# Kernel optimization log

Measured on AMD Instinct MI355X. Metric: run time of the kernel, lower is better.

The kernel has to match this reference:

```python
import jax, jax.numpy as jnp
import numpy as np

B, N, H = 4, 4096, 1024
NH, HD, M = 16, 64, 256
EPS = 1e-5


def gaussian_orthogonal(m, d, rng):
    # scaling=0: rows are orthogonal blocks scaled by norms of fresh gaussian rows
    blocks = []
    n_blocks = (m + d - 1) // d
    for _ in range(n_blocks):
        q, _ = np.linalg.qr(rng.standard_normal((d, d)))
        blocks.append(q.T)
    mat = np.concatenate(blocks, 0)[:m]
    multiplier = np.linalg.norm(rng.standard_normal((m, d)), axis=1)
    return (multiplier[:, None] * mat).astype(np.float32)


def setup_inputs():
    key = jax.random.key(0)
    keys = iter(jax.random.split(key, 24))
    rng = np.random.default_rng(0)

    def w(din, dout):
        return jax.random.normal(next(keys), (din, dout), jnp.float32) * 0.02

    inp = {
        'x': jax.random.normal(next(keys), (B, N, H), jnp.float32),
        'enc_outputs': jax.random.normal(next(keys), (B, N, H), jnp.float32),
    }
    for p in ('sa', 'ca'):
        for q in ('wq', 'wk', 'wv', 'wo'):
            inp[f'{p}_{q}'] = w(H, H)
            inp[f'{p}_b{q[1]}'] = jnp.zeros((H,), jnp.float32)
        inp[f'{p}_proj'] = jnp.asarray(gaussian_orthogonal(M, HD, rng))
    inp['ff_w1'] = w(H, 4 * H); inp['ff_b1'] = jnp.zeros((4 * H,), jnp.float32)
    inp['ff_w2'] = w(4 * H, H); inp['ff_b2'] = jnp.zeros((H,), jnp.float32)
    for i in (1, 2, 3):
        inp[f'ln{i}_g'] = jnp.ones((H,), jnp.float32)
        inp[f'ln{i}_b'] = jnp.zeros((H,), jnp.float32)
    return inp


def _split(t):
    b, n, _ = t.shape
    return t.reshape(b, n, NH, HD).transpose(0, 2, 1, 3)  # [b,h,n,d]


def _feat(data, proj):
    # FAVOR+ nonnegative softmax kernel features
    dn = HD ** -0.25
    dd = jnp.einsum('bhnd,md->bhnm', data * dn, proj)
    diag = 0.5 * (dn ** 2) * jnp.sum(data * data, -1)  # [b,h,n]
    dd = dd - diag[..., None] - jnp.max(dd, axis=-1, keepdims=True)
    return (M ** -0.5) * (jnp.exp(dd) + 1e-4)


def _attn(q, k, v, wq, bq, wk, bk, wv, bv, wo, bo, proj):
    b, n, _ = q.shape
    Q = _split(q @ wq + bq)
    K = _split(k @ wk + bk)
    V = _split(v @ wv + bv)
    Qp = _feat(Q, proj)  # [b,h,n,m]
    Kp = _feat(K, proj)
    denom = jnp.einsum('bhnm,bhm->bhn', Qp, Kp.sum(2))[..., None]
    ctx = jnp.einsum('bhnm,bhnd->bhmd', Kp, V)          # O(N) linear attention
    out = jnp.einsum('bhnm,bhmd->bhnd', Qp, ctx) / denom
    # faithful to torch .view(B,-1,hidden) WITHOUT head transpose-back
    out = out.reshape(b, -1, H)
    return out @ wo + bo


def _ln(x, g, b):
    mu = jnp.mean(x, -1, keepdims=True)
    var = jnp.mean((x - mu) ** 2, -1, keepdims=True)
    return (x - mu) / jnp.sqrt(var + EPS) * g + b


def reference(x, enc_outputs, sa_wq, sa_bq, sa_wk, sa_bk, sa_wv, sa_bv, sa_wo, sa_bo,
              sa_proj, ca_wq, ca_bq, ca_wk, ca_bk, ca_wv, ca_bv, ca_wo, ca_bo, ca_proj,
              ff_w1, ff_b1, ff_w2, ff_b2, ln1_g, ln1_b, ln2_g, ln2_b, ln3_g, ln3_b):
    h = _ln(x + _attn(x, x, x, sa_wq, sa_bq, sa_wk, sa_bk, sa_wv, sa_bv, sa_wo, sa_bo, sa_proj), ln1_g, ln1_b)
    h = _ln(h + _attn(h, enc_outputs, enc_outputs, ca_wq, ca_bq, ca_wk, ca_bk, ca_wv, ca_bv, ca_wo, ca_bo, ca_proj), ln2_g, ln2_b)
    ff = jax.nn.gelu(h @ ff_w1 + ff_b1, approximate=True) @ ff_w2 + ff_b2  # dropout prob 0 -> identity
    return _ln(h + ff, ln3_g, ln3_b)
```

## Files before the change

kernel.cpp:

```cpp
#include <hip/hip_runtime.h>
#include <hip/hip_bf16.h>

#define B_ 4
#define N_ 4096
#define H_ 1024
#define NH_ 16
#define HD_ 64
#define M_ 256

typedef __attribute__((ext_vector_type(8))) __bf16 bf16x8;
typedef __attribute__((ext_vector_type(4))) float f32x4;
typedef __attribute__((ext_vector_type(4))) unsigned int u32x4;

__device__ __forceinline__ float bf2f(unsigned short u) {
  union { unsigned int i; float f; } x; x.i = ((unsigned int)u) << 16; return x.f;
}
__device__ __forceinline__ unsigned short f2b(float f) {
  __hip_bfloat16 h = __float2bfloat16(f);
  return *(unsigned short*)&h;
}
__device__ __forceinline__ float gelu_f(float x) {
  const float c = 0.7978845608028654f;
  float t = tanhf(c * (x + 0.044715f * x * x * x));
  return 0.5f * x * (1.0f + t);
}

typedef __attribute__((address_space(3))) unsigned int as3_uint;
typedef const __attribute__((address_space(1))) unsigned int as1_uint;
__device__ __forceinline__ void gload16(const void* g, void* l) {
  __builtin_amdgcn_global_load_lds((as1_uint*)g, (as3_uint*)l, 16, 0, 0);
}

template<int ACT>
__launch_bounds__(256)
__global__ void gemm_mfma(const unsigned short* __restrict__ A, int lda,
                          const unsigned short* __restrict__ BT,
                          const float* __restrict__ bias,
                          unsigned short* __restrict__ C, int ldc, int K) {
  __shared__ __align__(16) char LDS[65536];

  const int tid = threadIdx.x;
  const int nwg = gridDim.x * gridDim.y;
  const int lin = blockIdx.y * gridDim.x + blockIdx.x;
  const int mm = (lin & 7) * (nwg >> 3) + (lin >> 3);
  const int bx = mm % gridDim.x, by = mm / gridDim.x;
  const int row0 = by * 128;
  const int col0 = bx * 128;

  const int w = tid >> 6, lane = tid & 63;
  const int wm = w >> 1, wn = w & 1;
  const int ln = lane & 15, hi = lane >> 4;
  const int rswz = (ln & 7) << 4;

  const int srow = w * 8 + (lane >> 3);
  const int schunk = ((lane & 7) ^ (lane >> 3)) * 8;
  const unsigned short* Ag = A + (long long)(row0 + srow) * lda + schunk;
  const unsigned short* Bg = BT + (long long)(col0 + srow) * K + schunk;
  const int ldsw = w * 1024;

  f32x4 acc[4][4];
#pragma unroll
  for (int i = 0; i < 4; ++i)
#pragma unroll
    for (int j = 0; j < 4; ++j) acc[i][j] = (f32x4){0.f, 0.f, 0.f, 0.f};

  auto STAGE = [&](int p, int k0) {
    char* dst = LDS + p * 32768 + ldsw;
#pragma unroll
    for (int i = 0; i < 4; ++i) {
      gload16(Ag + (long long)i * 32 * lda + k0, dst + i * 4096);
      gload16(Bg + (long long)i * 32 * K + k0, dst + 16384 + i * 4096);
    }
  };
  auto COMPUTE = [&](int p) {
    char* AsB = LDS + p * 32768;
    char* BsB = AsB + 16384;
#pragma unroll
    for (int kc = 0; kc < 2; ++kc) {
      const int koff = (kc * 64 + hi * 16) ^ rswz;
      bf16x8 av[4], bv[4];
#pragma unroll
      for (int i = 0; i < 4; ++i)
        av[i] = *(bf16x8*)(AsB + (wm * 64 + i * 16 + ln) * 128 + koff);
#pragma unroll
      for (int j = 0; j < 4; ++j)
        bv[j] = *(bf16x8*)(BsB + (wn * 64 + j * 16 + ln) * 128 + koff);
#pragma unroll
      for (int i = 0; i < 4; ++i)
#pragma unroll
        for (int j = 0; j < 4; ++j)
          acc[i][j] = __builtin_amdgcn_mfma_f32_16x16x32_bf16(av[i], bv[j], acc[i][j], 0, 0, 0);
    }
  };

  STAGE(0, 0);
  __syncthreads();
  int cur = 0;
  for (int k0 = 64; k0 < K; k0 += 64) {
    STAGE(cur ^ 1, k0);
    COMPUTE(cur);
    __syncthreads();
    cur ^= 1;
  }
  COMPUTE(cur);
  __syncthreads();

  char* SB = LDS;
#pragma unroll
  for (int j = 0; j < 4; ++j) {
    const int lcol = wn * 64 + j * 16 + ln;
    const float bj = bias ? bias[col0 + lcol] : 0.0f;
#pragma unroll
    for (int i = 0; i < 4; ++i) {
      const int rb_ = wm * 64 + i * 16 + hi * 4;
#pragma unroll
      for (int r = 0; r < 4; ++r) {
        float v = acc[i][j][r] + bj;
        if (ACT == 1) v = gelu_f(v);
        const int row = rb_ + r;
        *(unsigned short*)(SB + ((row * 256 + lcol * 2) ^ ((row & 7) << 4))) = f2b(v);
      }
    }
  }
  __syncthreads();
#pragma unroll
  for (int p = 0; p < 8; ++p) {
    const int idx = p * 256 + tid;
    const int row = idx >> 4, seg = idx & 15;
    u32x4 v = *(u32x4*)(SB + ((row * 256 + seg * 16) ^ ((row & 7) << 4)));
    __builtin_nontemporal_store(v, (u32x4*)(C + (long long)(row0 + row) * ldc + col0 + seg * 8));
  }
}

__launch_bounds__(256)
__global__ void ctxksum_mfma(const unsigned short* __restrict__ QKV,
                             const unsigned short* __restrict__ pjB,
                             float* __restrict__ ksumP,
                             float* __restrict__ ctxP) {
  __shared__ char Kt[8192];
  __shared__ char Vt[8192];
  __shared__ char Pt[32768];
  __shared__ float rmaxL[4][64];
  __shared__ float ssqL[64];
  const int z = blockIdx.z, b = z >> 4, hh = z & 15;
  const int sp = blockIdx.x;
  const int n0 = sp * 512;
  const unsigned short* Kg = QKV + (long long)(b * 4096) * 3072 + 1024 + hh * 64;
  const unsigned short* Vg = QKV + (long long)(b * 4096) * 3072 + 2048 + hh * 64;
  const int tid = threadIdx.x;
  const int w = tid >> 6, lane = tid & 63;
  const int ln = lane & 15, hi = lane >> 4;
  const int rswz = (ln & 7) << 4;

  f32x4 accC[4][4];
#pragma unroll
  for (int i = 0; i < 4; ++i)
#pragma unroll
    for (int j = 0; j < 4; ++j) accC[i][j] = (f32x4){0.f, 0.f, 0.f, 0.f};
  float cs[4] = {0.f, 0.f, 0.f, 0.f};

  for (int t = 0; t < 8; ++t) {
    const long long nt = n0 + t * 64;
    __syncthreads();
#pragma unroll
    for (int p = 0; p < 2; ++p) {
      int id = p * 256 + tid;
      int r = id >> 3, c = id & 7;
      gload16(Kg + (nt + r) * 3072 + ((c ^ (r & 7)) * 8), Kt + id * 16);
    }
    {
      int n = tid >> 2, d0 = (tid & 3) * 16;
      const unsigned short* src = Vg + (nt + n) * 3072 + d0;
      ushort4 v0 = *(const ushort4*)src;
      ushort4 v1 = *(const ushort4*)(src + 4);
      ushort4 v2 = *(const ushort4*)(src + 8);
      ushort4 v3 = *(const ushort4*)(src + 12);
      unsigned short vals[16] = {v0.x, v0.y, v0.z, v0.w, v1.x, v1.y, v1.z, v1.w,
                                 v2.x, v2.y, v2.z, v2.w, v3.x, v3.y, v3.z, v3.w};
#pragma unroll
      for (int e = 0; e < 16; ++e) {
        int d = d0 + e;
        *(unsigned short*)(Vt + ((d * 128 + n * 2) ^ ((d & 7) << 4))) = vals[e];
      }
    }
    __syncthreads();

    f32x4 accF[4][4];
#pragma unroll
    for (int i = 0; i < 4; ++i)
#pragma unroll
      for (int j = 0; j < 4; ++j) accF[i][j] = (f32x4){0.f, 0.f, 0.f, 0.f};
#pragma unroll
    for (int kc = 0; kc < 2; ++kc) {
      const int koff = (kc * 64 + hi * 16) ^ rswz;
      bf16x8 av[4], bq[4];
#pragma unroll
      for (int i = 0; i < 4; ++i)
        av[i] = *(bf16x8*)(Kt + (i * 16 + ln) * 128 + koff);
#pragma unroll
      for (int j = 0; j < 4; ++j)
        bq[j] = *(const bf16x8*)(pjB + (w * 64 + j * 16 + ln) * 64 + kc * 32 + hi * 8);
#pragma unroll
      for (int i = 0; i < 4; ++i)
#pragma unroll
        for (int j = 0; j < 4; ++j)
          accF[i][j] = __builtin_amdgcn_mfma_f32_16x16x32_bf16(av[i], bq[j], accF[i][j], 0, 0, 0);
    }

#pragma unroll
    for (int i = 0; i < 4; ++i)
#pragma unroll
      for (int r = 0; r < 4; ++r) {
        float m = fmaxf(fmaxf(accF[i][0][r], accF[i][1][r]), fmaxf(accF[i][2][r], accF[i][3][r]));
        m = fmaxf(m, __shfl_xor(m, 1, 64));
        m = fmaxf(m, __shfl_xor(m, 2, 64));
        m = fmaxf(m, __shfl_xor(m, 4, 64));
        m = fmaxf(m, __shfl_xor(m, 8, 64));
        if (ln == 0) rmaxL[w][i * 16 + hi * 4 + r] = m;
      }
    {
      int r = tid >> 2, q = tid & 3;
      int b0 = (r * 128 + q * 32) ^ ((r & 7) << 4);
      int b1 = (r * 128 + q * 32 + 16) ^ ((r & 7) << 4);
      u32x4 x0 = *(u32x4*)(Kt + b0);
      u32x4 x1 = *(u32x4*)(Kt + b1);
      float s = 0.f;
#pragma unroll
      for (int e = 0; e < 4; ++e) {
        float a0 = bf2f((unsigned short)(x0[e] & 0xffff)), a1 = bf2f((unsigned short)(x0[e] >> 16));
        float a2 = bf2f((unsigned short)(x1[e] & 0xffff)), a3 = bf2f((unsigned short)(x1[e] >> 16));
        s += a0 * a0 + a1 * a1 + a2 * a2 + a3 * a3;
      }
      s += __shfl_xor(s, 1, 64);
      s += __shfl_xor(s, 2, 64);
      if (q == 0) ssqL[r] = s;
    }
    __syncthreads();

    float base[4][4];
#pragma unroll
    for (int i = 0; i < 4; ++i)
#pragma unroll
      for (int r = 0; r < 4; ++r) {
        int row = i * 16 + hi * 4 + r;
        base[i][r] = 0.0625f * ssqL[row] +
                     fmaxf(fmaxf(rmaxL[0][row], rmaxL[1][row]), fmaxf(rmaxL[2][row], rmaxL[3][row]));
      }
#pragma unroll
    for (int i = 0; i < 4; ++i)
#pragma unroll
      for (int j = 0; j < 4; ++j) {
        ushort4 pk;
        pk.x = f2b(0.0625f * (expf(accF[i][j][0] - base[i][0]) + 1e-4f));
        pk.y = f2b(0.0625f * (expf(accF[i][j][1] - base[i][1]) + 1e-4f));
        pk.z = f2b(0.0625f * (expf(accF[i][j][2] - base[i][2]) + 1e-4f));
        pk.w = f2b(0.0625f * (expf(accF[i][j][3] - base[i][3]) + 1e-4f));
        cs[j] += bf2f(pk.x) + bf2f(pk.y) + bf2f(pk.z) + bf2f(pk.w);
        int m = w * 64 + j * 16 + ln;
        *(ushort4*)(Pt + ((m * 128 + i * 32 + hi * 8) ^ ((m & 7) << 4))) = pk;
      }
    __syncthreads();

#pragma unroll
    for (int kc = 0; kc < 2; ++kc) {
      const int koff = (kc * 64 + hi * 16) ^ rswz;
      bf16x8 am[4], bv[4];
#pragma unroll
      for (int i = 0; i < 4; ++i)
        am[i] = *(bf16x8*)(Pt + (w * 64 + i * 16 + ln) * 128 + koff);
#pragma unroll
      for (int j = 0; j < 4; ++j)
        bv[j] = *(bf16x8*)(Vt + (j * 16 + ln) * 128 + koff);
#pragma unroll
      for (int i = 0; i < 4; ++i)
#pragma unroll
        for (int j = 0; j < 4; ++j)
          accC[i][j] = __builtin_amdgcn_mfma_f32_16x16x32_bf16(am[i], bv[j], accC[i][j], 0, 0, 0);
    }
  }

#pragma unroll
  for (int j = 0; j < 4; ++j) {
    cs[j] += __shfl_xor(cs[j], 16, 64);
    cs[j] += __shfl_xor(cs[j], 32, 64);
  }
  if (hi == 0) {
#pragma unroll
    for (int j = 0; j < 4; ++j)
      ksumP[((long long)z * 8 + sp) * 256 + w * 64 + j * 16 + ln] = cs[j];
  }

  float* ctxPs = ctxP + ((long long)z * 8 + sp) * 16384;
#pragma unroll
  for (int dh = 0; dh < 2; ++dh) {
    __syncthreads();
#pragma unroll
    for (int i = 0; i < 4; ++i)
#pragma unroll
      for (int jj = 0; jj < 2; ++jj) {
        int j = dh * 2 + jj;
#pragma unroll
        for (int r = 0; r < 4; ++r) {
          int m = w * 64 + i * 16 + hi * 4 + r;
          int dl = jj * 16 + ln;
          *(float*)(Pt + ((m * 128 + dl * 4) ^ ((m & 7) << 4))) = accC[i][j][r];
        }
      }
    __syncthreads();
#pragma unroll
    for (int p = 0; p < 8; ++p) {
      int idx = p * 256 + tid;
      int row = idx >> 3, seg = idx & 7;
      u32x4 v = *(u32x4*)(Pt + ((row * 128 + seg * 16) ^ ((row & 7) << 4)));
      __builtin_nontemporal_store(v, (u32x4*)(ctxPs + dh * 8192 + row * 32 + seg * 4));
    }
  }
}

__launch_bounds__(256)
__global__ void ctx_fin(const float* __restrict__ ctxP, const float* __restrict__ ksumP,
                        unsigned short* __restrict__ ctxbf, float* __restrict__ ksumF) {
  __shared__ float acc[16384];
  const int z = blockIdx.x;
  const int tid = threadIdx.x;
  const float* base = ctxP + (long long)z * 8 * 16384;
  for (int i = tid; i < 16384; i += 256) {
    float s = 0.f;
#pragma unroll
    for (int q = 0; q < 8; ++q) s += base[(long long)q * 16384 + i];
    acc[i] = s;
  }
  {
    const float* kb = ksumP + (long long)z * 8 * 256;
    float s = 0.f;
#pragma unroll
    for (int q = 0; q < 8; ++q) s += kb[q * 256 + tid];
    ksumF[z * 256 + tid] = s;
  }
  __syncthreads();
  unsigned short* dst = ctxbf + (long long)z * 16384;
  for (int cc = tid; cc < 2048; cc += 256) {
    int mh = cc >> 10, rem = cc & 1023, d = rem >> 4, cl = rem & 15;
    int m0 = mh * 128 + cl * 8;
    int dh = d >> 5, dl = d & 31;
    ushort4 o0, o1;
    o0.x = f2b(acc[dh * 8192 + (m0 + 0) * 32 + dl]);
    o0.y = f2b(acc[dh * 8192 + (m0 + 1) * 32 + dl]);
    o0.z = f2b(acc[dh * 8192 + (m0 + 2) * 32 + dl]);
    o0.w = f2b(acc[dh * 8192 + (m0 + 3) * 32 + dl]);
    o1.x = f2b(acc[dh * 8192 + (m0 + 4) * 32 + dl]);
    o1.y = f2b(acc[dh * 8192 + (m0 + 5) * 32 + dl]);
    o1.z = f2b(acc[dh * 8192 + (m0 + 6) * 32 + dl]);
    o1.w = f2b(acc[dh * 8192 + (m0 + 7) * 32 + dl]);
    unsigned short* p = dst + (long long)mh * 8192 + (d * 16 + (cl ^ (d & 7))) * 8;
    *(ushort4*)p = o0;
    *(ushort4*)(p + 4) = o1;
  }
}

__launch_bounds__(256)
__global__ void ao_fused(const unsigned short* __restrict__ QKV,
                         const unsigned short* __restrict__ pjB,
                         const float* __restrict__ ksum,
                         const unsigned short* __restrict__ ctxbf,
                         unsigned short* __restrict__ AO) {
  __shared__ char Qt[8192];
  __shared__ char Ps[32768];
  __shared__ char Ch[32768];
  __shared__ float rmaxL[4][64];
  __shared__ float ssqL[64];
  __shared__ float dprt[4][64];
  __shared__ float denomS[64];
  const int z = blockIdx.z, b = z >> 4, hh = z & 15;
  const int n0 = blockIdx.x * 64;
  const unsigned short* Qg = QKV + (long long)(b * 4096) * 3072 + hh * 64;
  const int tid = threadIdx.x;
  const int w = tid >> 6, lane = tid & 63;
  const int ln = lane & 15, hi = lane >> 4;
  const int rswz = (ln & 7) << 4;

#pragma unroll
  for (int p = 0; p < 8; ++p) {
    int id = p * 256 + tid;
    gload16(ctxbf + (long long)z * 16384 + id * 8, Ch + id * 16);
  }
#pragma unroll
  for (int p = 0; p < 2; ++p) {
    int id = p * 256 + tid;
    int r = id >> 3, c = id & 7;
    gload16(Qg + (long long)(n0 + r) * 3072 + ((c ^ (r & 7)) * 8), Qt + id * 16);
  }
  __syncthreads();

  f32x4 accF[4][4];
#pragma unroll
  for (int i = 0; i < 4; ++i)
#pragma unroll
    for (int j = 0; j < 4; ++j) accF[i][j] = (f32x4){0.f, 0.f, 0.f, 0.f};
#pragma unroll
  for (int kc = 0; kc < 2; ++kc) {
    const int koff = (kc * 64 + hi * 16) ^ rswz;
    bf16x8 av[4], bq[4];
#pragma unroll
    for (int i = 0; i < 4; ++i)
      av[i] = *(bf16x8*)(Qt + (i * 16 + ln) * 128 + koff);
#pragma unroll
    for (int j = 0; j < 4; ++j)
      bq[j] = *(const bf16x8*)(pjB + (w * 64 + j * 16 + ln) * 64 + kc * 32 + hi * 8);
#pragma unroll
    for (int i = 0; i < 4; ++i)
#pragma unroll
      for (int j = 0; j < 4; ++j)
        accF[i][j] = __builtin_amdgcn_mfma_f32_16x16x32_bf16(av[i], bq[j], accF[i][j], 0, 0, 0);
  }

#pragma unroll
  for (int i = 0; i < 4; ++i)
#pragma unroll
    for (int r = 0; r < 4; ++r) {
      float m = fmaxf(fmaxf(accF[i][0][r], accF[i][1][r]), fmaxf(accF[i][2][r], accF[i][3][r]));
      m = fmaxf(m, __shfl_xor(m, 1, 64));
      m = fmaxf(m, __shfl_xor(m, 2, 64));
      m = fmaxf(m, __shfl_xor(m, 4, 64));
      m = fmaxf(m, __shfl_xor(m, 8, 64));
      if (ln == 0) rmaxL[w][i * 16 + hi * 4 + r] = m;
    }
  {
    int r = tid >> 2, q = tid & 3;
    int b0 = (r * 128 + q * 32) ^ ((r & 7) << 4);
    int b1 = (r * 128 + q * 32 + 16) ^ ((r & 7) << 4);
    u32x4 x0 = *(u32x4*)(Qt + b0);
    u32x4 x1 = *(u32x4*)(Qt + b1);
    float s = 0.f;
#pragma unroll
    for (int e = 0; e < 4; ++e) {
      float a0 = bf2f((unsigned short)(x0[e] & 0xffff)), a1 = bf2f((unsigned short)(x0[e] >> 16));
      float a2 = bf2f((unsigned short)(x1[e] & 0xffff)), a3 = bf2f((unsigned short)(x1[e] >> 16));
      s += a0 * a0 + a1 * a1 + a2 * a2 + a3 * a3;
    }
    s += __shfl_xor(s, 1, 64);
    s += __shfl_xor(s, 2, 64);
    if (q == 0) ssqL[r] = s;
  }
  __syncthreads();

  float ks[4];
#pragma unroll
  for (int j = 0; j < 4; ++j) ks[j] = ksum[z * 256 + w * 64 + j * 16 + ln];
#pragma unroll
  for (int i = 0; i < 4; ++i)
#pragma unroll
    for (int r = 0; r < 4; ++r) {
      int n = i * 16 + hi * 4 + r;
      float base = 0.0625f * ssqL[n] +
                   fmaxf(fmaxf(rmaxL[0][n], rmaxL[1][n]), fmaxf(rmaxL[2][n], rmaxL[3][n]));
      float dp = 0.f;
#pragma unroll
      for (int j = 0; j < 4; ++j) {
        float v = 0.0625f * (expf(accF[i][j][r] - base) + 1e-4f);
        unsigned short vb = f2b(v);
        int m = w * 64 + j * 16 + ln;
        *(unsigned short*)(Ps + n * 512 + ((m * 2) ^ ((n & 7) << 4))) = vb;
        dp += bf2f(vb) * ks[j];
      }
      dp += __shfl_xor(dp, 1, 64);
      dp += __shfl_xor(dp, 2, 64);
      dp += __shfl_xor(dp, 4, 64);
      dp += __shfl_xor(dp, 8, 64);
      if (ln == 0) dprt[w][n] = dp;
    }
  __syncthreads();
  if (tid < 64) denomS[tid] = dprt[0][tid] + dprt[1][tid] + dprt[2][tid] + dprt[3][tid];

  f32x4 accO[4];
#pragma unroll
  for (int j = 0; j < 4; ++j) accO[j] = (f32x4){0.f, 0.f, 0.f, 0.f};
#pragma unroll
  for (int mh = 0; mh < 2; ++mh) {
#pragma unroll
    for (int ms = 0; ms < 4; ++ms) {
      const int koff = (ms * 64 + hi * 16);
      bf16x8 ap = *(bf16x8*)(Ps + (w * 16 + ln) * 512 + ((mh * 256 + koff) ^ rswz));
      bf16x8 bc[4];
#pragma unroll
      for (int j = 0; j < 4; ++j)
        bc[j] = *(bf16x8*)(Ch + mh * 16384 + (j * 16 + ln) * 256 + (koff ^ rswz));
#pragma unroll
      for (int j = 0; j < 4; ++j)
        accO[j] = __builtin_amdgcn_mfma_f32_16x16x32_bf16(ap, bc[j], accO[j], 0, 0, 0);
    }
  }
  __syncthreads();

  float inv[4];
#pragma unroll
  for (int r = 0; r < 4; ++r) inv[r] = 1.0f / denomS[w * 16 + hi * 4 + r];
  char* Ct = Qt;
#pragma unroll
  for (int j = 0; j < 4; ++j)
#pragma unroll
    for (int r = 0; r < 4; ++r) {
      int n = w * 16 + hi * 4 + r;
      int d = j * 16 + ln;
      *(unsigned short*)(Ct + ((n * 128 + d * 2) ^ ((n & 7) << 4))) = f2b(accO[j][r] * inv[r]);
    }
  __syncthreads();
#pragma unroll
  for (int p = 0; p < 2; ++p) {
    int idx = p * 256 + tid;
    int row = idx >> 3, seg = idx & 7;
    u32x4 v = *(u32x4*)(Ct + ((row * 128 + seg * 16) ^ ((row & 7) << 4)));
    *(u32x4*)(AO + (long long)(b * 4096 + n0 + row) * 1024 + hh * 64 + seg * 8) = v;
  }
}

__launch_bounds__(256)
__global__ void wt_cvt(const float* __restrict__ in, unsigned short* __restrict__ out,
                       int K, int N) {
  __shared__ float t[32][33];
  int k0 = blockIdx.y * 32, n0 = blockIdx.x * 32;
  int tx = threadIdx.x & 31, ty = threadIdx.x >> 5;
  for (int r = ty; r < 32; r += 8) t[r][tx] = in[(long long)(k0 + r) * N + n0 + tx];
  __syncthreads();
  for (int r = ty; r < 32; r += 8) out[(long long)(n0 + r) * K + k0 + tx] = f2b(t[tx][r]);
}

__launch_bounds__(256)
__global__ void projB_cvt(const float* __restrict__ proj, unsigned short* __restrict__ out) {
  int i = blockIdx.x * 256 + threadIdx.x;
  out[i] = f2b(0.35355339059327373f * proj[i]);
}

__launch_bounds__(256)
__global__ void bias_cat(const float* __restrict__ b0, const float* __restrict__ b1,
                         const float* __restrict__ b2, float* __restrict__ out) {
  int i = blockIdx.x * 256 + threadIdx.x;
  float v;
  if (i < 1024) v = b0[i];
  else if (i < 2048) v = b1[i - 1024];
  else v = b2[i - 2048];
  out[i] = v;
}

__launch_bounds__(256)
__global__ void cvt_bf16(const float* __restrict__ in, unsigned short* __restrict__ out,
                         long long n) {
  long long stride = (long long)gridDim.x * 1024;
  for (long long i = ((long long)blockIdx.x * 256 + threadIdx.x) * 4; i < n; i += stride) {
    float4 v = *(const float4*)&in[i];
    ushort4 o;
    o.x = f2b(v.x); o.y = f2b(v.y); o.z = f2b(v.z); o.w = f2b(v.w);
    *(ushort4*)&out[i] = o;
  }
}

__launch_bounds__(256)
__global__ void ln_k(const float* __restrict__ resf, const unsigned short* __restrict__ resb,
                     const unsigned short* __restrict__ po,
                     const float* __restrict__ g, const float* __restrict__ be,
                     float* __restrict__ outf, unsigned short* __restrict__ outb) {
  long long row = blockIdx.x;
  int t = threadIdx.x;
  float x0, x1, x2, x3;
  if (resf) {
    float4 va = ((const float4*)(resf + row * H_))[t];
    x0 = va.x; x1 = va.y; x2 = va.z; x3 = va.w;
  } else {
    ushort4 va = ((const ushort4*)(resb + row * H_))[t];
    x0 = bf2f(va.x); x1 = bf2f(va.y); x2 = bf2f(va.z); x3 = bf2f(va.w);
  }
  {
    ushort4 vp = ((const ushort4*)(po + row * H_))[t];
    x0 += bf2f(vp.x); x1 += bf2f(vp.y); x2 += bf2f(vp.z); x3 += bf2f(vp.w);
  }
  float s = x0 + x1 + x2 + x3;
  float q = x0 * x0 + x1 * x1 + x2 * x2 + x3 * x3;
#pragma unroll
  for (int m = 1; m < 64; m <<= 1) { s += __shfl_xor(s, m, 64); q += __shfl_xor(q, m, 64); }
  __shared__ float ssum[4], ssq[4];
  int w = t >> 6, lane = t & 63;
  if (lane == 0) { ssum[w] = s; ssq[w] = q; }
  __syncthreads();
  s = ssum[0] + ssum[1] + ssum[2] + ssum[3];
  q = ssq[0] + ssq[1] + ssq[2] + ssq[3];
  float mean = s * (1.0f / H_);
  float var = q * (1.0f / H_) - mean * mean;
  float rstd = rsqrtf(var + 1e-5f);
  float4 vg = ((const float4*)g)[t];
  float4 vbe = ((const float4*)be)[t];
  float o0 = (x0 - mean) * rstd * vg.x + vbe.x;
  float o1 = (x1 - mean) * rstd * vg.y + vbe.y;
  float o2 = (x2 - mean) * rstd * vg.z + vbe.z;
  float o3 = (x3 - mean) * rstd * vg.w + vbe.w;
  if (outf) {
    float4 o; o.x = o0; o.y = o1; o.z = o2; o.w = o3;
    ((float4*)(outf + row * H_))[t] = o;
  }
  if (outb) {
    ushort4 ob; ob.x = f2b(o0); ob.y = f2b(o1); ob.z = f2b(o2); ob.w = f2b(o3);
    ((ushort4*)(outb + row * H_))[t] = ob;
  }
}

extern "C" void kernel_launch(void* const* d_in, const int* in_sizes, int n_in,
                              void* d_out, int out_size, void* d_ws, size_t ws_size,
                              hipStream_t stream) {
  (void)in_sizes; (void)n_in; (void)out_size; (void)ws_size;
  const float* x      = (const float*)d_in[0];
  const float* enc    = (const float*)d_in[1];
  const float* sa_w[4] = {(const float*)d_in[2], (const float*)d_in[4], (const float*)d_in[6], (const float*)d_in[8]};
  const float* sa_b[4] = {(const float*)d_in[3], (const float*)d_in[5], (const float*)d_in[7], (const float*)d_in[9]};
  const float* sa_pj  = (const float*)d_in[10];
  const float* ca_w[4] = {(const float*)d_in[11], (const float*)d_in[13], (const float*)d_in[15], (const float*)d_in[17]};
  const float* ca_b[4] = {(const float*)d_in[12], (const float*)d_in[14], (const float*)d_in[16], (const float*)d_in[18]};
  const float* ca_pj  = (const float*)d_in[19];
  const float* ff_w1  = (const float*)d_in[20];
  const float* ff_b1  = (const float*)d_in[21];
  const float* ff_w2  = (const float*)d_in[22];
  const float* ff_b2  = (const float*)d_in[23];
  const float* ln1_g  = (const float*)d_in[24];
  const float* ln1_b  = (const float*)d_in[25];
  const float* ln2_g  = (const float*)d_in[26];
  const float* ln2_b  = (const float*)d_in[27];
  const float* ln3_g  = (const float*)d_in[28];
  const float* ln3_b  = (const float*)d_in[29];

  float* ws = (float*)d_ws;
  unsigned short* XB = (unsigned short*)(ws);
  unsigned short* EB = (unsigned short*)(ws + 8388608LL);
  unsigned short* QKVb = (unsigned short*)(ws + 16777216LL);
  unsigned short* PO = (unsigned short*)(ws + 41943040LL);
  float* ctxP = ws + 41943040LL;
  unsigned short* MIDB = PO;
  unsigned short* FO = (unsigned short*)(ws + 50331648LL);
  unsigned short* WTph = (unsigned short*)(ws + 52428800LL);
  unsigned short* pjB = (unsigned short*)(ws + 54525952LL);
  float* ksumP = ws + 54542336LL;
  float* ksumF = ws + 54673408LL;
  unsigned short* ctxbf = (unsigned short*)(ws + 55607296LL);
  float* biasC = ws + 56131584LL;

  unsigned short* ff1T = EB;
  unsigned short* ff2T = EB + 4194304LL;
  unsigned short* pjB_sa = pjB, *pjB_ca = pjB + 16384;

  dim3 blk(256, 1, 1);
  const int LDQ = 3072;

  projB_cvt<<<dim3(64), blk, 0, stream>>>(sa_pj, pjB_sa);
  projB_cvt<<<dim3(64), blk, 0, stream>>>(ca_pj, pjB_ca);
  cvt_bf16<<<dim3(2048), blk, 0, stream>>>(x, XB, 16777216LL);

  auto attn_core = [&](const unsigned short* pj, const float* wo_bias) {
    ctxksum_mfma<<<dim3(8, 1, 64), blk, 0, stream>>>(QKVb, pj, ksumP, ctxP);
    ctx_fin<<<dim3(64), blk, 0, stream>>>(ctxP, ksumP, ctxbf, ksumF);
    ao_fused<<<dim3(64, 1, 64), blk, 0, stream>>>(QKVb, pj, ksumF, ctxbf, EB);
    gemm_mfma<0><<<dim3(8, 128), blk, 0, stream>>>(EB, H_, WTph + 3145728, wo_bias, PO, H_, H_);
  };

  for (int i = 0; i < 4; ++i)
    wt_cvt<<<dim3(32, 32), blk, 0, stream>>>(sa_w[i], WTph + (long long)i * 1048576, H_, H_);
  bias_cat<<<dim3(12), blk, 0, stream>>>(sa_b[0], sa_b[1], sa_b[2], biasC);
  gemm_mfma<0><<<dim3(24, 128), blk, 0, stream>>>(XB, H_, WTph, biasC, QKVb, LDQ, H_);
  attn_core(pjB_sa, sa_b[3]);
  ln_k<<<dim3(16384), blk, 0, stream>>>(x, nullptr, PO, ln1_g, ln1_b, nullptr, XB);

  cvt_bf16<<<dim3(2048), blk, 0, stream>>>(enc, EB, 16777216LL);
  for (int i = 0; i < 4; ++i)
    wt_cvt<<<dim3(32, 32), blk, 0, stream>>>(ca_w[i], WTph + (long long)i * 1048576, H_, H_);
  bias_cat<<<dim3(8), blk, 0, stream>>>(ca_b[1], ca_b[2], nullptr, biasC);
  gemm_mfma<0><<<dim3(8, 128), blk, 0, stream>>>(XB, H_, WTph, ca_b[0], QKVb, LDQ, H_);
  gemm_mfma<0><<<dim3(16, 128), blk, 0, stream>>>(EB, H_, WTph + 1048576, biasC, QKVb + 1024, LDQ, H_);
  attn_core(pjB_ca, ca_b[3]);
  ln_k<<<dim3(16384), blk, 0, stream>>>(nullptr, XB, PO, ln2_g, ln2_b, nullptr, XB);

  wt_cvt<<<dim3(128, 32), blk, 0, stream>>>(ff_w1, ff1T, H_, 4096);
  wt_cvt<<<dim3(32, 128), blk, 0, stream>>>(ff_w2, ff2T, 4096, H_);
  for (int c = 0; c < 4; ++c) {
    const long long co = (long long)c * 4096 * H_;
    gemm_mfma<1><<<dim3(32, 32), blk, 0, stream>>>(XB + co, H_, ff1T, ff_b1, MIDB, 4096, H_);
    gemm_mfma<0><<<dim3(8, 32), blk, 0, stream>>>(MIDB, 4096, ff2T, ff_b2, FO, H_, 4096);
    ln_k<<<dim3(4096), blk, 0, stream>>>(nullptr, XB + co, FO, ln3_g, ln3_b,
                                         (float*)d_out + co, nullptr);
  }
}
```

Before: 1.533 ms.

## Double-buffer K/V tiles and hoist projection loads in ctx/ksum kernel

Adds a second LDS buffer for the K and V tiles in the context/key-sum kernel so the next tile's global loads are issued before the current tile's MFMA work. The V writes into LDS are deferred until after the feature computation, and the loop-top barrier is removed. Projection-matrix fragments are now loaded into registers once before the loop rather than on every tile. The key-sum also now accumulates the fp32 feature values instead of the bf16-rounded ones, which slightly changes numerics. The extra LDS buffers increase shared-memory use and register pressure, which may lower occupancy.

Result: no change. 1.533 ms (-0.0%).

```diff
diff --git a/kernel.cpp b/kernel.cpp
--- a/kernel.cpp
+++ b/kernel.cpp
@@ -137,14 +137,14 @@
                              const unsigned short* __restrict__ pjB,
                              float* __restrict__ ksumP,
                              float* __restrict__ ctxP) {
-  __shared__ char Kt[8192];
-  __shared__ char Vt[8192];
+  __shared__ char Kt[2][8192];
+  __shared__ char Vt[2][8192];
   __shared__ char Pt[32768];
   __shared__ float rmaxL[4][64];
   __shared__ float ssqL[64];
   const int z = blockIdx.z, b = z >> 4, hh = z & 15;
   const int sp = blockIdx.x;
-  const int n0 = sp * 512;
+  const long long n0 = sp * 512;
   const unsigned short* Kg = QKV + (long long)(b * 4096) * 3072 + 1024 + hh * 64;
   const unsigned short* Vg = QKV + (long long)(b * 4096) * 3072 + 2048 + hh * 64;
   const int tid = threadIdx.x;
@@ -152,38 +152,60 @@
   const int ln = lane & 15, hi = lane >> 4;
   const int rswz = (ln & 7) << 4;
 
-  f32x4 accC[4][4];
-#pragma unroll
-  for (int i = 0; i < 4; ++i)
-#pragma unroll
-    for (int j = 0; j < 4; ++j) accC[i][j] = (f32x4){0.f, 0.f, 0.f, 0.f};
-  float cs[4] = {0.f, 0.f, 0.f, 0.f};
-
-  for (int t = 0; t < 8; ++t) {
-    const long long nt = n0 + t * 64;
-    __syncthreads();
+  bf16x8 bq[2][4];
+#pragma unroll
+  for (int kc = 0; kc < 2; ++kc)
+#pragma unroll
+    for (int j = 0; j < 4; ++j)
+      bq[kc][j] = *(const bf16x8*)(pjB + (w * 64 + j * 16 + ln) * 64 + kc * 32 + hi * 8);
+
+  const int vn = tid >> 2, vd0 = (tid & 3) * 16;
+  ushort4 vr[4];
+  auto VLOAD = [&](long long nt) {
+    const unsigned short* src = Vg + (nt + vn) * 3072 + vd0;
+    vr[0] = *(const ushort4*)src;
+    vr[1] = *(const ushort4*)(src + 4);
+    vr[2] = *(const ushort4*)(src + 8);
+    vr[3] = *(const ushort4*)(src + 12);
+  };
+  auto VWRITE = [&](int buf) {
+    unsigned short vals[16] = {vr[0].x, vr[0].y, vr[0].z, vr[0].w,
+                               vr[1].x, vr[1].y, vr[1].z, vr[1].w,
+                               vr[2].x, vr[2].y, vr[2].z, vr[2].w,
+                               vr[3].x, vr[3].y, vr[3].z, vr[3].w};
+#pragma unroll
+    for (int e = 0; e < 16; ++e) {
+      int d = vd0 + e;
+      *(unsigned short*)(Vt[buf] + ((d * 128 + vn * 2) ^ ((d & 7) << 4))) = vals[e];
+    }
+  };
+  auto KSTAGE = [&](long long nt, int buf) {
 #pragma unroll
     for (int p = 0; p < 2; ++p) {
       int id = p * 256 + tid;
       int r = id >> 3, c = id & 7;
-      gload16(Kg + (nt + r) * 3072 + ((c ^ (r & 7)) * 8), Kt + id * 16);
-    }
-    {
-      int n = tid >> 2, d0 = (tid & 3) * 16;
-      const unsigned short* src = Vg + (nt + n) * 3072 + d0;
-      ushort4 v0 = *(const ushort4*)src;
-      ushort4 v1 = *(const ushort4*)(src + 4);
-      ushort4 v2 = *(const ushort4*)(src + 8);
-      ushort4 v3 = *(const ushort4*)(src + 12);
-      unsigned short vals[16] = {v0.x, v0.y, v0.z, v0.w, v1.x, v1.y, v1.z, v1.w,
-                                 v2.x, v2.y, v2.z, v2.w, v3.x, v3.y, v3.z, v3.w};
-#pragma unroll
-      for (int e = 0; e < 16; ++e) {
-        int d = d0 + e;
-        *(unsigned short*)(Vt + ((d * 128 + n * 2) ^ ((d & 7) << 4))) = vals[e];
-      }
-    }
-    __syncthreads();
+      gload16(Kg + (nt + r) * 3072 + ((c ^ (r & 7)) * 8), Kt[buf] + id * 16);
+    }
+  };
+
+  f32x4 accC[4][4];
+#pragma unroll
+  for (int i = 0; i < 4; ++i)
+#pragma unroll
+    for (int j = 0; j < 4; ++j) accC[i][j] = (f32x4){0.f, 0.f, 0.f, 0.f};
+  float cs[4] = {0.f, 0.f, 0.f, 0.f};
+
+  KSTAGE(n0, 0);
+  VLOAD(n0);
+  VWRITE(0);
+  __syncthreads();
+
+  for (int t = 0; t < 8; ++t) {
+    const int cur = t & 1;
+    if (t < 7) {
+      KSTAGE(n0 + (t + 1) * 64, cur ^ 1);
+      VLOAD(n0 + (t + 1) * 64);
+    }
 
     f32x4 accF[4][4];
 #pragma unroll
@@ -193,18 +215,15 @@
 #pragma unroll
     for (int kc = 0; kc < 2; ++kc) {
       const int koff = (kc * 64 + hi * 16) ^ rswz;
-      bf16x8 av[4], bq[4];
+      bf16x8 av[4];
 #pragma unroll
       for (int i = 0; i < 4; ++i)
-        av[i] = *(bf16x8*)(Kt + (i * 16 + ln) * 128 + koff);
-#pragma unroll
-      for (int j = 0; j < 4; ++j)
-        bq[j] = *(const bf16x8*)(pjB + (w * 64 + j * 16 + ln) * 64 + kc * 32 + hi * 8);
+        av[i] = *(bf16x8*)(Kt[cur] + (i * 16 + ln) * 128 + koff);
 #pragma unroll
       for (int i = 0; i < 4; ++i)
 #pragma unroll
         for (int j = 0; j < 4; ++j)
-          accF[i][j] = __builtin_amdgcn_mfma_f32_16x16x32_bf16(av[i], bq[j], accF[i][j], 0, 0, 0);
+          accF[i][j] = __builtin_amdgcn_mfma_f32_16x16x32_bf16(av[i], bq[kc][j], accF[i][j], 0, 0, 0);
     }
 
 #pragma unroll
@@ -222,8 +241,8 @@
       int r = tid >> 2, q = tid & 3;
       int b0 = (r * 128 + q * 32) ^ ((r & 7) << 4);
       int b1 = (r * 128 + q * 32 + 16) ^ ((r & 7) << 4);
-      u32x4 x0 = *(u32x4*)(Kt + b0);
-      u32x4 x1 = *(u32x4*)(Kt + b1);
+      u32x4 x0 = *(u32x4*)(Kt[cur] + b0);
+      u32x4 x1 = *(u32x4*)(Kt[cur] + b1);
       float s = 0.f;
 #pragma unroll
       for (int e = 0; e < 4; ++e) {
@@ -250,15 +269,17 @@
     for (int i = 0; i < 4; ++i)
 #pragma unroll
       for (int j = 0; j < 4; ++j) {
+        float v0 = 0.0625f * (expf(accF[i][j][0] - base[i][0]) + 1e-4f);
+        float v1 = 0.0625f * (expf(accF[i][j][1] - base[i][1]) + 1e-4f);
+        float v2 = 0.0625f * (expf(accF[i][j][2] - base[i][2]) + 1e-4f);
+        float v3 = 0.0625f * (expf(accF[i][j][3] - base[i][3]) + 1e-4f);
+        cs[j] += v0 + v1 + v2 + v3;
         ushort4 pk;
-        pk.x = f2b(0.0625f * (expf(accF[i][j][0] - base[i][0]) + 1e-4f));
-        pk.y = f2b(0.0625f * (expf(accF[i][j][1] - base[i][1]) + 1e-4f));
-        pk.z = f2b(0.0625f * (expf(accF[i][j][2] - base[i][2]) + 1e-4f));
-        pk.w = f2b(0.0625f * (expf(accF[i][j][3] - base[i][3]) + 1e-4f));
-        cs[j] += bf2f(pk.x) + bf2f(pk.y) + bf2f(pk.z) + bf2f(pk.w);
+        pk.x = f2b(v0); pk.y = f2b(v1); pk.z = f2b(v2); pk.w = f2b(v3);
         int m = w * 64 + j * 16 + ln;
         *(ushort4*)(Pt + ((m * 128 + i * 32 + hi * 8) ^ ((m & 7) << 4))) = pk;
       }
+    if (t < 7) VWRITE(cur ^ 1);
     __syncthreads();
 
 #pragma unroll
@@ -270,7 +291,7 @@
         am[i] = *(bf16x8*)(Pt + (w * 64 + i * 16 + ln) * 128 + koff);
 #pragma unroll
       for (int j = 0; j < 4; ++j)
-        bv[j] = *(bf16x8*)(Vt + (j * 16 + ln) * 128 + koff);
+        bv[j] = *(bf16x8*)(Vt[cur] + (j * 16 + ln) * 128 + koff);
 #pragma unroll
       for (int i = 0; i < 4; ++i)
 #pragma unroll
```
